# Optimization experiments

Measured on AMD Instinct MI355X. Metric: run time of the kernel, lower is better.

## Reference

```python
import jax, jax.numpy as jnp
import numpy as np

B, H, W, C = 4, 64, 64, 256
D = C // 8  # q/k projection dim


def setup_inputs() -> dict:
    key = jax.random.key(0)
    ks = jax.random.split(key, 5)
    scale = lambda fan_in: 1.0 / np.sqrt(fan_in)
    return {
        "x": jax.random.normal(ks[0], (B, H, W, C), dtype=jnp.float32),
        "wq": jax.random.normal(ks[1], (C, D), dtype=jnp.float32) * scale(C),
        "bq": jnp.zeros((D,), dtype=jnp.float32),
        "wk": jax.random.normal(ks[2], (C, D), dtype=jnp.float32) * scale(C),
        "bk": jnp.zeros((D,), dtype=jnp.float32),
        "wv": jax.random.normal(ks[3], (C, C), dtype=jnp.float32) * scale(C),
        "bv": jnp.zeros((C,), dtype=jnp.float32),
        "wo": jax.random.normal(ks[4], (C, C), dtype=jnp.float32) * scale(C),
        "bo": jnp.zeros((C,), dtype=jnp.float32),
    }


def reference(x, wq, bq, wk, bk, wv, bv, wo, bo):
    b, h, w, c = x.shape
    n = h * w
    xt = x.reshape(b, n, c)  # 1x1 conv == per-pixel linear over channels
    q = xt @ wq + bq                      # [b, n, d]
    k = xt @ wk + bk                      # [b, n, d]
    v = xt @ wv + bv                      # [b, n, c]
    scores = jnp.einsum("bnd,bmd->bnm", q, k) / jnp.sqrt(jnp.float32(k.shape[-1]))
    attn = jax.nn.softmax(scores, axis=-1)  # [b, n, n]
    attended = jnp.einsum("bnm,bmc->bnc", attn, v)  # [b, n, c]
    out = attended @ wo + bo
    return x + out.reshape(b, h, w, c)
```

## Files before the change

### kernel.cpp

```cpp
#include <hip/hip_runtime.h>
#include <math.h>

#define B_   4
#define N_   4096
#define C_   256
#define D_   32

typedef __attribute__((ext_vector_type(8))) short short8;
typedef __attribute__((ext_vector_type(4))) float f32x4;
typedef __attribute__((ext_vector_type(4))) unsigned short us4;

__device__ __forceinline__ unsigned short f2bf(float f) {
    unsigned int u = __float_as_uint(f);
    u = (u + 0x7FFFu + ((u >> 16) & 1u)) >> 16;
    return (unsigned short)u;
}
__device__ __forceinline__ unsigned short p2bf(float f) {
    return (unsigned short)((__float_as_uint(f) + 0x8000u) >> 16);
}
__device__ __forceinline__ float bf2f(unsigned short h) {
    return __uint_as_float(((unsigned int)h) << 16);
}

__device__ __forceinline__ void dma16(const unsigned short* g, unsigned short* l) {
    __builtin_amdgcn_global_load_lds(
        (const __attribute__((address_space(1))) unsigned int*)(uintptr_t)(g),
        (__attribute__((address_space(3))) unsigned int*)(unsigned int)(uintptr_t)(l),
        16, 0, 0);
}

__global__ __launch_bounds__(256) void prep_w_kernel(const float* __restrict__ wq,
                                                     const float* __restrict__ wk,
                                                     const float* __restrict__ wv,
                                                     const float* __restrict__ wo,
                                                     unsigned short* __restrict__ wqkvT,
                                                     unsigned short* __restrict__ woT) {
    int idx = blockIdx.x * 256 + threadIdx.x;
    if (idx < 320 * 256) {
        int n = idx >> 8, c = idx & 255;
        float v = (n < 32) ? wq[c * 32 + n]
                : (n < 64) ? wk[c * 32 + (n - 32)]
                           : wv[c * 256 + (n - 64)];
        wqkvT[idx] = f2bf(v);
    } else {
        int j = idx - 320 * 256;
        int n = j >> 8, c = j & 255;
        woT[j] = f2bf(wo[c * 256 + n]);
    }
}

__global__ __launch_bounds__(256) void qkv_gemm_kernel(const float* __restrict__ x,
        const unsigned short* __restrict__ wqkvT,
        const float* __restrict__ bq, const float* __restrict__ bk, const float* __restrict__ bv,
        unsigned short* __restrict__ qb, unsigned short* __restrict__ kb,
        unsigned short* __restrict__ vT) {
    const int tid = threadIdx.x;
    const int wave = tid >> 6, lane = tid & 63;
    const int quad = lane >> 4, li = lane & 15;
    const int rows0 = blockIdx.x * 32;
    const float kS = 0.17677669529663687f * 1.4426950408889634f;

    __shared__ __align__(16) unsigned short xs[32 * 264];

#pragma unroll
    for (int i = 0; i < 8; ++i) {
        int flat = i * 256 + tid;
        int row = flat >> 6, c4 = flat & 63;
        float4 f = *(const float4*)(x + (size_t)(rows0 + row) * 256 + c4 * 4);
        us4 o = { f2bf(f.x), f2bf(f.y), f2bf(f.z), f2bf(f.w) };
        *(us4*)&xs[row * 264 + c4 * 4] = o;
    }
    __syncthreads();

    const int rowt = wave & 1;
    const int nt0 = (wave >> 1) * 10;
    const int r0 = rows0 + rowt * 16;

    short8 A[8];
#pragma unroll
    for (int kc = 0; kc < 8; ++kc)
        A[kc] = *(const short8*)&xs[(rowt * 16 + li) * 264 + kc * 32 + quad * 8];

#pragma unroll
    for (int j = 0; j < 10; ++j) {
        const int nt = nt0 + j;
        f32x4 acc = {0.f, 0.f, 0.f, 0.f};
#pragma unroll
        for (int kc = 0; kc < 8; ++kc) {
            short8 Bf = *(const short8*)(wqkvT + (size_t)(nt * 16 + li) * 256 + kc * 32 + quad * 8);
            acc = __builtin_amdgcn_mfma_f32_16x16x32_bf16(A[kc], Bf, acc, 0, 0, 0);
        }
        int n = nt * 16 + li;
        float bias = (nt < 2) ? bq[n] : (nt < 4) ? bk[n - 32] : bv[n - 64];
        if (nt < 4) {
            unsigned short* dst = (nt < 2) ? qb : kb;
            float scl = (nt < 2) ? kS : 1.0f;
            int d = (nt < 2) ? n : (n - 32);
#pragma unroll
            for (int jj = 0; jj < 4; ++jj)
                dst[(size_t)(r0 + quad * 4 + jj) * 32 + d] = f2bf((acc[jj] + bias) * scl);
        } else {
            int c = n - 64;
            int p = r0 + quad * 4;
            int b = p >> 12, ni = p & 4095;
            us4 hv = { f2bf(acc[0] + bias), f2bf(acc[1] + bias),
                       f2bf(acc[2] + bias), f2bf(acc[3] + bias) };
            *(us4*)(vT + ((size_t)(b * 256 + c) * 4096 + ni)) = hv;
        }
    }
}

__global__ __launch_bounds__(256, 2) void attn_partial_kernel(
        const unsigned short* __restrict__ qb, const unsigned short* __restrict__ kb,
        const unsigned short* __restrict__ vT,
        unsigned short* __restrict__ Obf, float* __restrict__ ml) {
    const int tid = threadIdx.x;
    const int wave = tid >> 6, lane = tid & 63;
    const int quad = lane >> 4, li = lane & 15;
    const int by = blockIdx.y, sg = blockIdx.z;
    const int pw = blockIdx.x * 128 + wave * 32;
    const int key0 = sg * 1024;

    __shared__ __align__(16) unsigned short smem[21504];
    unsigned short* v0 = smem;
    unsigned short* v1 = smem + 8192;
    unsigned short* pw_ = smem + 16384 + wave * 1280;

    short8 a_q[2];
#pragma unroll
    for (int qf = 0; qf < 2; ++qf)
        a_q[qf] = *(const short8*)(qb + (size_t)(by * N_ + pw + qf * 16 + li) * 32 + quad * 8);

    const int o8 = lane >> 3, s8 = lane & 7;
    const int sp = s8 ^ o8;
    const int chl = sp >> 2, chk = sp & 3;
    auto stage = [&](int kt, unsigned short* buf) {
#pragma unroll
        for (int h = 0; h < 4; ++h) {
            int ch = ((h * 32 + wave * 8 + o8) << 1) + chl;
            const unsigned short* g = vT + (size_t)(by * 256 + ch) * 4096
                                        + key0 + kt * 32 + chk * 8;
            dma16(g, buf + (h * 256 + wave * 64) * 8);
        }
    };

    stage(0, v0);

    const f32x4 Z = {0.f, 0.f, 0.f, 0.f};
    f32x4 O[2][16];
#pragma unroll
    for (int qf = 0; qf < 2; ++qf)
#pragma unroll
        for (int ct = 0; ct < 16; ++ct) O[qf][ct] = Z;
    f32x4 lsum[2] = {Z, Z};
    short8 ones;
#pragma unroll
    for (int j = 0; j < 8; ++j) ones[j] = (short)0x3F80;

    short8 kf0, kf1;
    {
        const unsigned short* krow = kb + (size_t)(by * N_ + key0) * 32;
        kf0 = *(const short8*)(krow + li * 32 + quad * 8);
        kf1 = *(const short8*)(krow + (16 + li) * 32 + quad * 8);
    }

    const int voff = (li >> 1) * 64 + ((((li & 1) * 4 + quad) ^ ((li >> 1) & 7)) * 8);

    unsigned short* vc = v0;
    unsigned short* vn = v1;
#pragma unroll 1
    for (int kt = 0; kt < 32; ++kt) {
        __builtin_amdgcn_s_waitcnt(0x0f70);
        __syncthreads();

        short8 kn0 = kf0, kn1 = kf1;
        if (kt < 31) {
            stage(kt + 1, vn);
            const unsigned short* krow = kb + (size_t)(by * N_ + key0 + (kt + 1) * 32) * 32;
            kn0 = *(const short8*)(krow + li * 32 + quad * 8);
            kn1 = *(const short8*)(krow + (16 + li) * 32 + quad * 8);
        }

#pragma unroll
        for (int qf = 0; qf < 2; ++qf) {
            f32x4 s0 = __builtin_amdgcn_mfma_f32_16x16x32_bf16(a_q[qf], kf0, Z, 0, 0, 0);
            f32x4 s1 = __builtin_amdgcn_mfma_f32_16x16x32_bf16(a_q[qf], kf1, Z, 0, 0, 0);
#pragma unroll
            for (int r = 0; r < 4; ++r) {
                float p0 = __builtin_amdgcn_exp2f(s0[r]);
                float p1 = __builtin_amdgcn_exp2f(s1[r]);
                pw_[(qf * 16 + quad * 4 + r) * 40 + li]      = p2bf(p0);
                pw_[(qf * 16 + quad * 4 + r) * 40 + 16 + li] = p2bf(p1);
            }
        }

        short8 ap0 = *(const short8*)(pw_ + li * 40 + quad * 8);
        short8 ap1 = *(const short8*)(pw_ + (16 + li) * 40 + quad * 8);
        lsum[0] = __builtin_amdgcn_mfma_f32_16x16x32_bf16(ap0, ones, lsum[0], 0, 0, 0);
        lsum[1] = __builtin_amdgcn_mfma_f32_16x16x32_bf16(ap1, ones, lsum[1], 0, 0, 0);
#pragma unroll
        for (int ct = 0; ct < 16; ++ct) {
            short8 bv8 = *(const short8*)(vc + ct * 512 + voff);
            O[0][ct] = __builtin_amdgcn_mfma_f32_16x16x32_bf16(ap0, bv8, O[0][ct], 0, 0, 0);
            O[1][ct] = __builtin_amdgcn_mfma_f32_16x16x32_bf16(ap1, bv8, O[1][ct], 0, 0, 0);
        }

        kf0 = kn0; kf1 = kn1;
        unsigned short* t = vc; vc = vn; vn = t;
    }

    __syncthreads();
    unsigned short* att = smem + wave * 4224;
    const int srow = lane & 15, scc = (lane >> 4) * 64;
#pragma unroll
    for (int qf = 0; qf < 2; ++qf) {
#pragma unroll
        for (int ct = 0; ct < 16; ++ct)
#pragma unroll
            for (int r = 0; r < 4; ++r)
                att[(quad * 4 + r) * 264 + ct * 16 + li] = f2bf(O[qf][ct][r]);
        const int pbase = by * N_ + pw + qf * 16;
        unsigned short* dst = Obf + ((size_t)(pbase + srow) * 4 + sg) * 256 + scc;
#pragma unroll
        for (int h = 0; h < 8; ++h)
            *(short8*)(dst + h * 8) = *(const short8*)(att + srow * 264 + scc + h * 8);
        if (li == 0) {
#pragma unroll
            for (int r = 0; r < 4; ++r) {
                int pp = pbase + quad * 4 + r;
                ml[pp * 4 + sg] = lsum[qf][r];
            }
        }
    }
}

__global__ __launch_bounds__(256) void merge_proj_kernel(
        const unsigned short* __restrict__ Obf, const float* __restrict__ ml,
        const unsigned short* __restrict__ woT, const float* __restrict__ x,
        const float* __restrict__ bo, float* __restrict__ out) {
    const int tid = threadIdx.x;
    const int px = blockIdx.x * 16;
    __shared__ __align__(16) unsigned short att[16 * 264];

    {
        const int row = tid >> 4, chc = tid & 15;
        const int p = px + row;
        float lt = ml[p * 4] + ml[p * 4 + 1] + ml[p * 4 + 2] + ml[p * 4 + 3];
        float inv = 1.0f / lt;
        float acc[16];
#pragma unroll
        for (int i = 0; i < 16; ++i) acc[i] = 0.f;
#pragma unroll
        for (int s = 0; s < 4; ++s) {
            const unsigned short* src = Obf + (size_t)(p * 4 + s) * 256 + chc * 16;
            short8 v0 = *(const short8*)(src);
            short8 v1 = *(const short8*)(src + 8);
#pragma unroll
            for (int jj = 0; jj < 8; ++jj) {
                acc[jj]     += bf2f((unsigned short)v0[jj]);
                acc[8 + jj] += bf2f((unsigned short)v1[jj]);
            }
        }
        short8 o0, o1;
#pragma unroll
        for (int jj = 0; jj < 8; ++jj) {
            o0[jj] = (short)f2bf(acc[jj] * inv);
            o1[jj] = (short)f2bf(acc[8 + jj] * inv);
        }
        *(short8*)&att[row * 264 + chc * 16]     = o0;
        *(short8*)&att[row * 264 + chc * 16 + 8] = o1;
    }
    __syncthreads();

    const int wave = tid >> 6, lane = tid & 63;
    const int quad = lane >> 4, li = lane & 15;
    short8 bfr[8];
#pragma unroll
    for (int kc = 0; kc < 8; ++kc)
        bfr[kc] = *(const short8*)&att[li * 264 + kc * 32 + quad * 8];
#pragma unroll
    for (int mt = 0; mt < 4; ++mt) {
        const int mtg = wave * 4 + mt;
        f32x4 acc = {0.f, 0.f, 0.f, 0.f};
#pragma unroll
        for (int kc = 0; kc < 8; ++kc) {
            short8 aw = *(const short8*)(woT + (size_t)(mtg * 16 + li) * 256 + kc * 32 + quad * 8);
            acc = __builtin_amdgcn_mfma_f32_16x16x32_bf16(aw, bfr[kc], acc, 0, 0, 0);
        }
        const int pg = px + li;
        const float4 xv  = *(const float4*)(x  + (size_t)pg * 256 + mtg * 16 + quad * 4);
        const float4 bv4 = *(const float4*)(bo + mtg * 16 + quad * 4);
        float4 o4;
        o4.x = acc[0] + xv.x + bv4.x;
        o4.y = acc[1] + xv.y + bv4.y;
        o4.z = acc[2] + xv.z + bv4.z;
        o4.w = acc[3] + xv.w + bv4.w;
        *(float4*)(out + (size_t)pg * 256 + mtg * 16 + quad * 4) = o4;
    }
}

extern "C" void kernel_launch(void* const* d_in, const int* in_sizes, int n_in,
                              void* d_out, int out_size, void* d_ws, size_t ws_size,
                              hipStream_t stream) {
    const float* x  = (const float*)d_in[0];
    const float* wq = (const float*)d_in[1];
    const float* bq = (const float*)d_in[2];
    const float* wk = (const float*)d_in[3];
    const float* bk = (const float*)d_in[4];
    const float* wv = (const float*)d_in[5];
    const float* bv = (const float*)d_in[6];
    const float* wo = (const float*)d_in[7];
    const float* bo = (const float*)d_in[8];
    float* out = (float*)d_out;

    char* ws = (char*)d_ws;
    unsigned short* wqkvT = (unsigned short*)(ws);
    unsigned short* woT   = (unsigned short*)(ws +   163840);
    unsigned short* qb    = (unsigned short*)(ws +   294912);
    unsigned short* kb    = (unsigned short*)(ws +  1343488);
    unsigned short* vT    = (unsigned short*)(ws +  2392064);
    unsigned short* Obf   = (unsigned short*)(ws + 10780672);
    float*          ml    = (float*)         (ws + 44335104);

    hipLaunchKernelGGL(prep_w_kernel,      dim3(576),       dim3(256), 0, stream, wq, wk, wv, wo, wqkvT, woT);
    hipLaunchKernelGGL(qkv_gemm_kernel,    dim3(512),       dim3(256), 0, stream, x, wqkvT, bq, bk, bv, qb, kb, vT);
    hipLaunchKernelGGL(attn_partial_kernel,dim3(32, 4, 4),  dim3(256), 0, stream, qb, kb, vT, Obf, ml);
    hipLaunchKernelGGL(merge_proj_kernel,  dim3(1024),      dim3(256), 0, stream, Obf, ml, woT, x, bo, out);
}
```

Baseline: 177.9 us.

## Triple-buffer V staging, remap blocks per XCD, and raise MFMA priority

The attention kernel now stages V tiles two iterations ahead using three LDS buffers. It replaces the full waitcnt plus __syncthreads with a partial vmcnt wait and a bare s_barrier, so more global loads stay in flight. The 3D grid becomes a flat 512-block grid, remapped so each XCD handles the same batch/key-segment groups, which should improve L2 locality for K/V. s_setprio is raised around the MFMA block. In exchange, LDS per block grows, which could reduce occupancy, and the hand-counted vmcnt values must match the exact number of outstanding loads.

```diff
diff --git a/kernel.cpp b/kernel.cpp
--- a/kernel.cpp
+++ b/kernel.cpp
@@ -117,14 +117,17 @@
     const int tid = threadIdx.x;
     const int wave = tid >> 6, lane = tid & 63;
     const int quad = lane >> 4, li = lane & 15;
-    const int by = blockIdx.y, sg = blockIdx.z;
-    const int pw = blockIdx.x * 128 + wave * 32;
+
+    const int bid = blockIdx.x;
+    const int xcd = bid & 7, jj_ = bid >> 3;
+    const int qt = jj_ & 31;
+    const int g = (xcd << 1) | (jj_ >> 5);
+    const int by = g >> 2, sg = g & 3;
+    const int pw = qt * 128 + wave * 32;
     const int key0 = sg * 1024;
 
-    __shared__ __align__(16) unsigned short smem[21504];
-    unsigned short* v0 = smem;
-    unsigned short* v1 = smem + 8192;
-    unsigned short* pw_ = smem + 16384 + wave * 1280;
+    __shared__ __align__(16) unsigned short smem[29696];
+    unsigned short* pw_ = smem + 24576 + wave * 1280;
 
     short8 a_q[2];
 #pragma unroll
@@ -138,48 +141,51 @@
 #pragma unroll
         for (int h = 0; h < 4; ++h) {
             int ch = ((h * 32 + wave * 8 + o8) << 1) + chl;
-            const unsigned short* g = vT + (size_t)(by * 256 + ch) * 4096
-                                        + key0 + kt * 32 + chk * 8;
-            dma16(g, buf + (h * 256 + wave * 64) * 8);
+            const unsigned short* g2 = vT + (size_t)(by * 256 + ch) * 4096
+                                         + key0 + kt * 32 + chk * 8;
+            dma16(g2, buf + (h * 256 + wave * 64) * 8);
         }
     };
 
-    stage(0, v0);
-
-    const f32x4 Z = {0.f, 0.f, 0.f, 0.f};
-    f32x4 O[2][16];
-#pragma unroll
-    for (int qf = 0; qf < 2; ++qf)
-#pragma unroll
-        for (int ct = 0; ct < 16; ++ct) O[qf][ct] = Z;
-    f32x4 lsum[2] = {Z, Z};
-    short8 ones;
-#pragma unroll
-    for (int j = 0; j < 8; ++j) ones[j] = (short)0x3F80;
-
+    stage(0, smem);
     short8 kf0, kf1;
     {
         const unsigned short* krow = kb + (size_t)(by * N_ + key0) * 32;
         kf0 = *(const short8*)(krow + li * 32 + quad * 8);
         kf1 = *(const short8*)(krow + (16 + li) * 32 + quad * 8);
     }
+    stage(1, smem + 8192);
+
+    const f32x4 Z = {0.f, 0.f, 0.f, 0.f};
+    f32x4 O[2][16];
+#pragma unroll
+    for (int qf = 0; qf < 2; ++qf)
+#pragma unroll
+        for (int ct = 0; ct < 16; ++ct) O[qf][ct] = Z;
+    f32x4 lsum[2] = {Z, Z};
+    short8 ones;
+#pragma unroll
+    for (int j = 0; j < 8; ++j) ones[j] = (short)0x3F80;
 
     const int voff = (li >> 1) * 64 + ((((li & 1) * 4 + quad) ^ ((li >> 1) & 7)) * 8);
 
-    unsigned short* vc = v0;
-    unsigned short* vn = v1;
+    unsigned short* vc  = smem;
+    unsigned short* vn1 = smem + 8192;
+    unsigned short* vn2 = smem + 16384;
 #pragma unroll 1
     for (int kt = 0; kt < 32; ++kt) {
-        __builtin_amdgcn_s_waitcnt(0x0f70);
-        __syncthreads();
+        if (kt == 0)      asm volatile("s_waitcnt vmcnt(4)" ::: "memory");
+        else if (kt < 31) asm volatile("s_waitcnt vmcnt(6)" ::: "memory");
+        else              asm volatile("s_waitcnt vmcnt(2)" ::: "memory");
+        __builtin_amdgcn_s_barrier();
 
         short8 kn0 = kf0, kn1 = kf1;
         if (kt < 31) {
-            stage(kt + 1, vn);
             const unsigned short* krow = kb + (size_t)(by * N_ + key0 + (kt + 1) * 32) * 32;
             kn0 = *(const short8*)(krow + li * 32 + quad * 8);
             kn1 = *(const short8*)(krow + (16 + li) * 32 + quad * 8);
         }
+        if (kt < 30) stage(kt + 2, vn2);
 
 #pragma unroll
         for (int qf = 0; qf < 2; ++qf) {
@@ -196,6 +202,7 @@
 
         short8 ap0 = *(const short8*)(pw_ + li * 40 + quad * 8);
         short8 ap1 = *(const short8*)(pw_ + (16 + li) * 40 + quad * 8);
+        __builtin_amdgcn_s_setprio(1);
         lsum[0] = __builtin_amdgcn_mfma_f32_16x16x32_bf16(ap0, ones, lsum[0], 0, 0, 0);
         lsum[1] = __builtin_amdgcn_mfma_f32_16x16x32_bf16(ap1, ones, lsum[1], 0, 0, 0);
 #pragma unroll
@@ -204,9 +211,10 @@
             O[0][ct] = __builtin_amdgcn_mfma_f32_16x16x32_bf16(ap0, bv8, O[0][ct], 0, 0, 0);
             O[1][ct] = __builtin_amdgcn_mfma_f32_16x16x32_bf16(ap1, bv8, O[1][ct], 0, 0, 0);
         }
+        __builtin_amdgcn_s_setprio(0);
 
         kf0 = kn0; kf1 = kn1;
-        unsigned short* t = vc; vc = vn; vn = t;
+        unsigned short* t = vc; vc = vn1; vn1 = vn2; vn2 = t;
     }
 
     __syncthreads();
@@ -324,6 +332,6 @@
 
     hipLaunchKernelGGL(prep_w_kernel,      dim3(576),       dim3(256), 0, stream, wq, wk, wv, wo, wqkvT, woT);
     hipLaunchKernelGGL(qkv_gemm_kernel,    dim3(512),       dim3(256), 0, stream, x, wqkvT, bq, bk, bv, qb, kb, vT);
-    hipLaunchKernelGGL(attn_partial_kernel,dim3(32, 4, 4),  dim3(256), 0, stream, qb, kb, vT, Obf, ml);
+    hipLaunchKernelGGL(attn_partial_kernel,dim3(512),       dim3(256), 0, stream, qb, kb, vT, Obf, ml);
     hipLaunchKernelGGL(merge_proj_kernel,  dim3(1024),      dim3(256), 0, stream, Obf, ml, woT, x, bo, out);
 }
```

Result: no change. 177.4 us (-0.3%).

## Split keys into eight segments with XCD-aware block mapping and higher occupancy

Applied to the files above, without the earlier changes.

The attention kernel now takes the number of key segments as a parameter and uses 8 segments (512 keys each) when the workspace is large enough, doubling the grid to 1024 blocks. Block IDs are remapped so each XCD handles contiguous batch/segment groups, which should improve L2 reuse of K/V. Launch bounds are raised to 3 blocks per CU. The cost is twice as much partial-output traffic and more reduction work in the merge kernel, plus possible register spilling under the tighter bound.

```diff
diff --git a/kernel.cpp b/kernel.cpp
--- a/kernel.cpp
+++ b/kernel.cpp
@@ -110,16 +110,24 @@
     }
 }
 
-__global__ __launch_bounds__(256, 2) void attn_partial_kernel(
+__global__ __launch_bounds__(256, 3) void attn_partial_kernel(
         const unsigned short* __restrict__ qb, const unsigned short* __restrict__ kb,
         const unsigned short* __restrict__ vT,
-        unsigned short* __restrict__ Obf, float* __restrict__ ml) {
+        unsigned short* __restrict__ Obf, float* __restrict__ ml,
+        int nseg, int segshift) {
     const int tid = threadIdx.x;
     const int wave = tid >> 6, lane = tid & 63;
     const int quad = lane >> 4, li = lane & 15;
-    const int by = blockIdx.y, sg = blockIdx.z;
-    const int pw = blockIdx.x * 128 + wave * 32;
-    const int key0 = sg * 1024;
+
+    const int bid = blockIdx.x;
+    const int xcd = bid & 7, jj_ = bid >> 3;
+    const int qt = jj_ & 31;
+    const int g = xcd * (nseg >> 1) + (jj_ >> 5);
+    const int by = g >> segshift, sg = g & (nseg - 1);
+    const int pw = qt * 128 + wave * 32;
+    const int kseg = N_ >> segshift;
+    const int key0 = sg * kseg;
+    const int ktmax = kseg >> 5;
 
     __shared__ __align__(16) unsigned short smem[21504];
     unsigned short* v0 = smem;
@@ -138,9 +146,9 @@
 #pragma unroll
         for (int h = 0; h < 4; ++h) {
             int ch = ((h * 32 + wave * 8 + o8) << 1) + chl;
-            const unsigned short* g = vT + (size_t)(by * 256 + ch) * 4096
-                                        + key0 + kt * 32 + chk * 8;
-            dma16(g, buf + (h * 256 + wave * 64) * 8);
+            const unsigned short* g2 = vT + (size_t)(by * 256 + ch) * 4096
+                                         + key0 + kt * 32 + chk * 8;
+            dma16(g2, buf + (h * 256 + wave * 64) * 8);
         }
     };
 
@@ -169,12 +177,12 @@
     unsigned short* vc = v0;
     unsigned short* vn = v1;
 #pragma unroll 1
-    for (int kt = 0; kt < 32; ++kt) {
+    for (int kt = 0; kt < ktmax; ++kt) {
         __builtin_amdgcn_s_waitcnt(0x0f70);
         __syncthreads();
 
         short8 kn0 = kf0, kn1 = kf1;
-        if (kt < 31) {
+        if (kt < ktmax - 1) {
             stage(kt + 1, vn);
             const unsigned short* krow = kb + (size_t)(by * N_ + key0 + (kt + 1) * 32) * 32;
             kn0 = *(const short8*)(krow + li * 32 + quad * 8);
@@ -220,7 +228,7 @@
             for (int r = 0; r < 4; ++r)
                 att[(quad * 4 + r) * 264 + ct * 16 + li] = f2bf(O[qf][ct][r]);
         const int pbase = by * N_ + pw + qf * 16;
-        unsigned short* dst = Obf + ((size_t)(pbase + srow) * 4 + sg) * 256 + scc;
+        unsigned short* dst = Obf + ((size_t)(pbase + srow) * nseg + sg) * 256 + scc;
 #pragma unroll
         for (int h = 0; h < 8; ++h)
             *(short8*)(dst + h * 8) = *(const short8*)(att + srow * 264 + scc + h * 8);
@@ -228,7 +236,7 @@
 #pragma unroll
             for (int r = 0; r < 4; ++r) {
                 int pp = pbase + quad * 4 + r;
-                ml[pp * 4 + sg] = lsum[qf][r];
+                ml[pp * nseg + sg] = lsum[qf][r];
             }
         }
     }
@@ -237,7 +245,7 @@
 __global__ __launch_bounds__(256) void merge_proj_kernel(
         const unsigned short* __restrict__ Obf, const float* __restrict__ ml,
         const unsigned short* __restrict__ woT, const float* __restrict__ x,
-        const float* __restrict__ bo, float* __restrict__ out) {
+        const float* __restrict__ bo, float* __restrict__ out, int nseg) {
     const int tid = threadIdx.x;
     const int px = blockIdx.x * 16;
     __shared__ __align__(16) unsigned short att[16 * 264];
@@ -245,14 +253,15 @@
     {
         const int row = tid >> 4, chc = tid & 15;
         const int p = px + row;
-        float lt = ml[p * 4] + ml[p * 4 + 1] + ml[p * 4 + 2] + ml[p * 4 + 3];
+        float lt = 0.f;
+        for (int s = 0; s < nseg; ++s) lt += ml[p * nseg + s];
         float inv = 1.0f / lt;
         float acc[16];
 #pragma unroll
         for (int i = 0; i < 16; ++i) acc[i] = 0.f;
-#pragma unroll
-        for (int s = 0; s < 4; ++s) {
-            const unsigned short* src = Obf + (size_t)(p * 4 + s) * 256 + chc * 16;
+#pragma unroll 4
+        for (int s = 0; s < nseg; ++s) {
+            const unsigned short* src = Obf + (size_t)(p * nseg + s) * 256 + chc * 16;
             short8 v0 = *(const short8*)(src);
             short8 v1 = *(const short8*)(src + 8);
 #pragma unroll
@@ -313,6 +322,10 @@
     const float* bo = (const float*)d_in[8];
     float* out = (float*)d_out;
 
+    const int use8 = (ws_size >= 78413824u) ? 1 : 0;
+    const int nseg = use8 ? 8 : 4;
+    const int segshift = use8 ? 3 : 2;
+
     char* ws = (char*)d_ws;
     unsigned short* wqkvT = (unsigned short*)(ws);
     unsigned short* woT   = (unsigned short*)(ws +   163840);
@@ -320,10 +333,11 @@
     unsigned short* kb    = (unsigned short*)(ws +  1343488);
     unsigned short* vT    = (unsigned short*)(ws +  2392064);
     unsigned short* Obf   = (unsigned short*)(ws + 10780672);
-    float*          ml    = (float*)         (ws + 44335104);
-
-    hipLaunchKernelGGL(prep_w_kernel,      dim3(576),       dim3(256), 0, stream, wq, wk, wv, wo, wqkvT, woT);
-    hipLaunchKernelGGL(qkv_gemm_kernel,    dim3(512),       dim3(256), 0, stream, x, wqkvT, bq, bk, bv, qb, kb, vT);
-    hipLaunchKernelGGL(attn_partial_kernel,dim3(32, 4, 4),  dim3(256), 0, stream, qb, kb, vT, Obf, ml);
-    hipLaunchKernelGGL(merge_proj_kernel,  dim3(1024),      dim3(256), 0, stream, Obf, ml, woT, x, bo, out);
-}
+    float*          ml    = (float*)(ws + 10780672
+                                     + (size_t)16384 * nseg * 256 * 2);
+
+    hipLaunchKernelGGL(prep_w_kernel,      dim3(576),        dim3(256), 0, stream, wq, wk, wv, wo, wqkvT, woT);
+    hipLaunchKernelGGL(qkv_gemm_kernel,    dim3(512),        dim3(256), 0, stream, x, wqkvT, bq, bk, bv, qb, kb, vT);
+    hipLaunchKernelGGL(attn_partial_kernel,dim3(128 * nseg), dim3(256), 0, stream, qb, kb, vT, Obf, ml, nseg, segshift);
+    hipLaunchKernelGGL(merge_proj_kernel,  dim3(1024),       dim3(256), 0, stream, Obf, ml, woT, x, bo, out, nseg);
+}
```

Result: slower. 265.5 us (+49.3%).

## Stage V transpose through LDS and remap attention blocks per XCD

Applied to the files above, without the earlier changes.

The QKV GEMM now writes its transposed V tile into shared memory and then emits coalesced 16-byte row stores to vT, replacing scattered 8-byte strided global writes. The attention kernel moves to a 1D grid of 512 blocks and maps block IDs so that each XCD handles whole (batch, key-split) groups. This keeps the same K/V slices within one XCD's L2. The cost is extra LDS traffic and two added barriers in the GEMM.

```diff
diff --git a/kernel.cpp b/kernel.cpp
--- a/kernel.cpp
+++ b/kernel.cpp
@@ -58,9 +58,10 @@
     const int wave = tid >> 6, lane = tid & 63;
     const int quad = lane >> 4, li = lane & 15;
     const int rows0 = blockIdx.x * 32;
+    const int bb = rows0 >> 12, ni0 = rows0 & 4095;
     const float kS = 0.17677669529663687f * 1.4426950408889634f;
 
-    __shared__ __align__(16) unsigned short xs[32 * 264];
+    __shared__ __align__(16) unsigned short sbuf[10240];
 
 #pragma unroll
     for (int i = 0; i < 8; ++i) {
@@ -68,7 +69,7 @@
         int row = flat >> 6, c4 = flat & 63;
         float4 f = *(const float4*)(x + (size_t)(rows0 + row) * 256 + c4 * 4);
         us4 o = { f2bf(f.x), f2bf(f.y), f2bf(f.z), f2bf(f.w) };
-        *(us4*)&xs[row * 264 + c4 * 4] = o;
+        *(us4*)&sbuf[row * 264 + c4 * 4] = o;
     }
     __syncthreads();
 
@@ -79,7 +80,8 @@
     short8 A[8];
 #pragma unroll
     for (int kc = 0; kc < 8; ++kc)
-        A[kc] = *(const short8*)&xs[(rowt * 16 + li) * 264 + kc * 32 + quad * 8];
+        A[kc] = *(const short8*)&sbuf[(rowt * 16 + li) * 264 + kc * 32 + quad * 8];
+    __syncthreads();
 
 #pragma unroll
     for (int j = 0; j < 10; ++j) {
@@ -101,12 +103,20 @@
                 dst[(size_t)(r0 + quad * 4 + jj) * 32 + d] = f2bf((acc[jj] + bias) * scl);
         } else {
             int c = n - 64;
-            int p = r0 + quad * 4;
-            int b = p >> 12, ni = p & 4095;
+            int lp = rowt * 16 + quad * 4;
             us4 hv = { f2bf(acc[0] + bias), f2bf(acc[1] + bias),
                        f2bf(acc[2] + bias), f2bf(acc[3] + bias) };
-            *(us4*)(vT + ((size_t)(b * 256 + c) * 4096 + ni)) = hv;
-        }
+            *(us4*)&sbuf[c * 40 + lp] = hv;
+        }
+    }
+    __syncthreads();
+
+    {
+        const unsigned short* src = sbuf + tid * 40;
+        unsigned short* dstv = vT + ((size_t)(bb * 256 + tid) * 4096 + ni0);
+#pragma unroll
+        for (int k2 = 0; k2 < 4; ++k2)
+            *(short8*)(dstv + k2 * 8) = *(const short8*)(src + k2 * 8);
     }
 }
 
@@ -117,8 +127,13 @@
     const int tid = threadIdx.x;
     const int wave = tid >> 6, lane = tid & 63;
     const int quad = lane >> 4, li = lane & 15;
-    const int by = blockIdx.y, sg = blockIdx.z;
-    const int pw = blockIdx.x * 128 + wave * 32;
+
+    const int bid = blockIdx.x;
+    const int xcd = bid & 7, jj_ = bid >> 3;
+    const int qt = jj_ & 31;
+    const int g = (xcd << 1) | (jj_ >> 5);
+    const int by = g >> 2, sg = g & 3;
+    const int pw = qt * 128 + wave * 32;
     const int key0 = sg * 1024;
 
     __shared__ __align__(16) unsigned short smem[21504];
@@ -138,9 +153,9 @@
 #pragma unroll
         for (int h = 0; h < 4; ++h) {
             int ch = ((h * 32 + wave * 8 + o8) << 1) + chl;
-            const unsigned short* g = vT + (size_t)(by * 256 + ch) * 4096
-                                        + key0 + kt * 32 + chk * 8;
-            dma16(g, buf + (h * 256 + wave * 64) * 8);
+            const unsigned short* g2 = vT + (size_t)(by * 256 + ch) * 4096
+                                         + key0 + kt * 32 + chk * 8;
+            dma16(g2, buf + (h * 256 + wave * 64) * 8);
         }
     };
 
@@ -322,8 +337,8 @@
     unsigned short* Obf   = (unsigned short*)(ws + 10780672);
     float*          ml    = (float*)         (ws + 44335104);
 
-    hipLaunchKernelGGL(prep_w_kernel,      dim3(576),       dim3(256), 0, stream, wq, wk, wv, wo, wqkvT, woT);
-    hipLaunchKernelGGL(qkv_gemm_kernel,    dim3(512),       dim3(256), 0, stream, x, wqkvT, bq, bk, bv, qb, kb, vT);
-    hipLaunchKernelGGL(attn_partial_kernel,dim3(32, 4, 4),  dim3(256), 0, stream, qb, kb, vT, Obf, ml);
-    hipLaunchKernelGGL(merge_proj_kernel,  dim3(1024),      dim3(256), 0, stream, Obf, ml, woT, x, bo, out);
-}
+    hipLaunchKernelGGL(prep_w_kernel,      dim3(576),  dim3(256), 0, stream, wq, wk, wv, wo, wqkvT, woT);
+    hipLaunchKernelGGL(qkv_gemm_kernel,    dim3(512),  dim3(256), 0, stream, x, wqkvT, bq, bk, bv, qb, kb, vT);
+    hipLaunchKernelGGL(attn_partial_kernel,dim3(512),  dim3(256), 0, stream, qb, kb, vT, Obf, ml);
+    hipLaunchKernelGGL(merge_proj_kernel,  dim3(1024), dim3(256), 0, stream, Obf, ml, woT, x, bo, out);
+}
```

Measured after the change: 176.3 us. No clear change (-0.9%).
